# Optimization experiments

Hardware: AMD Instinct MI355X
Metric: run time of the kernel (lower is better)

## Reference

```python
import jax, jax.numpy as jnp
import numpy as np

K_PRED = 6
SCORE_TEMPERATURE = 0.5
NMS_THRESH = np.array([2.5, 1.0, 1.5], dtype=np.float32)  # [veh, ped, cyc] meters
SUPPRESSED_SCORE = 0.001


def setup_inputs() -> dict:
    key = jax.random.key(0)
    k0, k1, k2, k3 = jax.random.split(key, 4)
    D, S, A, P, T = 1, 64, 128, 6, 80  # n_decoder, n_scene, n_agent, n_pred, n_step_future
    pred_valid = jnp.ones((S, A), dtype=bool)
    pred_conf = jax.random.normal(k0, (D, S, A, P), dtype=jnp.float32)
    # scale positions to realistic meters so distances straddle the NMS thresholds
    pred_pos = jax.random.normal(k1, (D, S, A, P, T, 2), dtype=jnp.float32) * 10.0
    pred_yaw_bbox = jax.random.normal(k2, (D, S, A, P, T, 1), dtype=jnp.float32)
    type_idx = jax.random.randint(k3, (S, A), 0, 3)
    ref_type = jax.nn.one_hot(type_idx, 3, dtype=jnp.float32)
    return {
        'pred_valid': pred_valid,
        'pred_conf': pred_conf,
        'pred_pos': pred_pos,
        'pred_yaw_bbox': pred_yaw_bbox,
        'ref_type': ref_type,
    }


def _nms_one_agent(scores, within, valid):
    # scores: [K], within: [K, K] bool, valid: scalar bool
    order = jnp.argsort(-scores)  # descending, computed once on original scores

    def step(cur, k):
        # suppress k if any other prediction within distance has a (currently) higher score
        mask = within[k] & (cur > cur[k])
        new_val = jnp.where(jnp.any(mask), jnp.asarray(SUPPRESSED_SCORE, cur.dtype), cur[k])
        return cur.at[k].set(new_val), None

    out, _ = jax.lax.scan(step, scores, order)
    return jnp.where(valid, out, scores)


_nms = jax.vmap(jax.vmap(_nms_one_agent))  # over scene, agent


def reference(pred_valid, pred_conf, pred_pos, pred_yaw_bbox, ref_type):
    D, S, A, P, T, _ = pred_pos.shape
    K = D * P
    # [n_scene, n_agent, k_pred, n_step, 2]
    trajs = jnp.moveaxis(pred_pos, 0, 2).reshape(S, A, K, T, 2)
    scores = jax.nn.softmax(pred_conf, axis=-1)
    scores = jnp.moveaxis(scores, 0, 2).reshape(S, A, K)
    scores = scores / jnp.sum(scores, axis=-1, keepdims=True)

    # mpa_nms: per-agent-type distance threshold
    thresh = jnp.einsum('sat,t->sa', ref_type, jnp.asarray(NMS_THRESH))[:, :, None, None]
    # use_ade=True: mean pairwise distance over time -> [S, A, K, K]
    diff = trajs[:, :, :, None] - trajs[:, :, None, :]          # [S,A,K,K,T,2]
    within_dist = jnp.mean(jnp.linalg.norm(diff, axis=-1), axis=-1) < thresh
    scores = _nms(scores, within_dist, pred_valid)
    scores = scores / jnp.sum(scores, axis=-1, keepdims=True)

    # score temperature
    scores = jax.nn.softmax(jnp.log(scores) / SCORE_TEMPERATURE, axis=-1)

    waymo_trajs = jnp.moveaxis(trajs, 3, 1)                      # [S, T, A, K, 2]
    waymo_scores = scores                                        # [S, A, K]
    waymo_valid = jnp.broadcast_to(pred_valid[:, None, :], (S, T, A))
    yaw_bbox = jnp.moveaxis(pred_yaw_bbox, 0, 2).reshape(S, A, K, T, 1)
    waymo_yaw_bbox = jnp.moveaxis(yaw_bbox, 3, 1)                # [S, T, A, K, 1]
    return waymo_valid, waymo_trajs, waymo_scores, waymo_yaw_bbox
```

## Files before the change

### kernel.cpp

```cpp
#include <hip/hip_runtime.h>
#include <hip/hip_bf16.h>

#define NS 64
#define NA 128
#define NK 6
#define NT 80
#define THREADS 512
#define TILE_A 8
#define NROWS (TILE_A * NK)

#define OFF_TRAJ   655360
#define OFF_SCORE  (655360 + 7864320)
#define OFF_YAW    (655360 + 7864320 + 49152)

#define PSTRIDE 82
#define YSTRIDE 84

typedef float nfloat4 __attribute__((ext_vector_type(4)));

__global__ __launch_bounds__(THREADS) void waymo_post_kernel(
    const int*    __restrict__ validIn,
    const float*  __restrict__ confIn,
    const float2* __restrict__ posIn,
    const float*  __restrict__ yawIn,
    const float*  __restrict__ typeIn,
    float*        __restrict__ out)
{
    const int g   = blockIdx.x;
    const int tid = threadIdx.x;
    const int s   = g >> 4;
    const int a0  = (g & 15) * TILE_A;

    __shared__ float2 sPos[NROWS * PSTRIDE];
    __shared__ float  sYaw[NROWS * YSTRIDE];

    const size_t sa0 = (size_t)s * NA + a0;
    const float2* pbase = posIn + sa0 * (NK * NT);
    const float*  ybase = yawIn + sa0 * (NK * NT);

    for (int i = tid; i < NROWS * (NT / 2); i += THREADS) {
        int r = i / 40, q = i - r * 40;
        nfloat4 v = *(const nfloat4*)(pbase + (size_t)r * NT + 2 * q);
        *(nfloat4*)&sPos[r * PSTRIDE + 2 * q] = v;
    }
    for (int i = tid; i < NROWS * (NT / 4); i += THREADS) {
        int r = i / 20, m = i - r * 20;
        nfloat4 v = *(const nfloat4*)(ybase + (size_t)r * NT + 4 * m);
        *(nfloat4*)&sYaw[r * YSTRIDE + 4 * m] = v;
    }
    __syncthreads();

    float* outSc = out + OFF_SCORE;

    if (tid < 256) {
        const int la   = tid >> 5;
        const int lane = tid & 31;
        const int a    = a0 + la;
        const int p    = lane >> 1;
        const int half = lane & 1;

        const size_t sa = (size_t)s * NA + a;
        const float th = 2.5f * typeIn[sa * 3 + 0]
                       + 1.0f * typeIn[sa * 3 + 1]
                       + 1.5f * typeIn[sa * 3 + 2];

        int pi, pj;
        if      (p < 5)  { pi = 0; pj = p + 1; }
        else if (p < 9)  { pi = 1; pj = p - 3; }
        else if (p < 12) { pi = 2; pj = p - 6; }
        else if (p < 14) { pi = 3; pj = p - 8; }
        else             { pi = 4; pj = 5;     }

        const int rI = la * NK + pi, rJ = la * NK + pj;
        float dsum = 0.f;
        for (int t = half * 40; t < half * 40 + 40; ++t) {
            float2 u = sPos[rI * PSTRIDE + t];
            float2 v = sPos[rJ * PSTRIDE + t];
            float dx = u.x - v.x, dy = u.y - v.y;
            dsum += sqrtf(dx * dx + dy * dy);
        }
        dsum += __shfl_xor(dsum, 1);
        const bool within = (dsum / 80.0f) < th;
        const bool predb  = (half == 0) && (p < 15) && within;
        unsigned long long bal = __ballot(predb);
        unsigned mask32 = (unsigned)(bal >> (tid & 32));

        if (lane == 0) {
            float c[NK];
            float mx = -3e38f;
            for (int q = 0; q < NK; ++q) { c[q] = confIn[sa * NK + q]; mx = fmaxf(mx, c[q]); }
            float ssum = 0.f;
            for (int q = 0; q < NK; ++q) { c[q] = expf(c[q] - mx); ssum += c[q]; }
            for (int q = 0; q < NK; ++q) c[q] /= ssum;
            ssum = 0.f;
            for (int q = 0; q < NK; ++q) ssum += c[q];
            for (int q = 0; q < NK; ++q) c[q] /= ssum;

            int ord[NK]; bool used[NK];
            for (int q = 0; q < NK; ++q) used[q] = false;
            for (int st = 0; st < NK; ++st) {
                int best = 0; float bv = -3e38f;
                for (int q = 0; q < NK; ++q)
                    if (!used[q] && c[q] > bv) { bv = c[q]; best = q; }
                used[best] = true; ord[st] = best;
            }

            float cur[NK];
            for (int q = 0; q < NK; ++q) cur[q] = c[q];

            if (validIn[sa] != 0) {
                for (int st = 0; st < NK; ++st) {
                    int k = ord[st];
                    float ck = cur[k];
                    bool any = false;
                    for (int j = 0; j < NK; ++j) {
                        if (j == k) continue;
                        int lo = j < k ? j : k;
                        int hi = j < k ? k : j;
                        int pidx = lo * 5 - (lo * (lo - 1)) / 2 + (hi - lo - 1);
                        if (((mask32 >> (2 * pidx)) & 1u) && (cur[j] > ck)) any = true;
                    }
                    if (any) cur[k] = 0.001f;
                }
            }

            float tsum = 0.f;
            for (int q = 0; q < NK; ++q) tsum += cur[q];
            float w[NK]; float wsum = 0.f;
            for (int q = 0; q < NK; ++q) {
                float qq = cur[q] / tsum;
                w[q] = qq * qq; wsum += w[q];
            }
            for (int q = 0; q < NK; ++q) outSc[sa * NK + q] = w[q] / wsum;
        }
    }

    nfloat4* trajOut = (nfloat4*)(out + OFF_TRAJ);
    for (int o = tid; o < NT * 24; o += THREADS) {
        int t = o / 24, j = o - (o / 24) * 24;
        float2 u = sPos[(2 * j + 0) * PSTRIDE + t];
        float2 w = sPos[(2 * j + 1) * PSTRIDE + t];
        nfloat4 v{u.x, u.y, w.x, w.y};
        size_t f4 = (((size_t)(s * NT + t) * NA + a0) * NK) >> 1;
        __builtin_nontemporal_store(v, trajOut + f4 + j);
    }
    nfloat4* yawOut = (nfloat4*)(out + OFF_YAW);
    for (int o = tid; o < NT * 12; o += THREADS) {
        int t = o / 12, j = o - (o / 12) * 12;
        nfloat4 v{sYaw[(4 * j + 0) * YSTRIDE + t],
                  sYaw[(4 * j + 1) * YSTRIDE + t],
                  sYaw[(4 * j + 2) * YSTRIDE + t],
                  sYaw[(4 * j + 3) * YSTRIDE + t]};
        size_t f4 = (((size_t)(s * NT + t) * NA + a0) * NK) >> 2;
        __builtin_nontemporal_store(v, yawOut + f4 + j);
    }
    if (tid < 160) {
        int t = tid >> 1, q = tid & 1;
        nfloat4 v;
        v.x = (validIn[sa0 + 4 * q + 0] != 0) ? 1.0f : 0.0f;
        v.y = (validIn[sa0 + 4 * q + 1] != 0) ? 1.0f : 0.0f;
        v.z = (validIn[sa0 + 4 * q + 2] != 0) ? 1.0f : 0.0f;
        v.w = (validIn[sa0 + 4 * q + 3] != 0) ? 1.0f : 0.0f;
        size_t f4 = ((size_t)(s * NT + t) * NA + a0) >> 2;
        __builtin_nontemporal_store(v, (nfloat4*)out + f4 + q);
    }
}

extern "C" void kernel_launch(void* const* d_in, const int* in_sizes, int n_in,
                              void* d_out, int out_size, void* d_ws, size_t ws_size,
                              hipStream_t stream) {
    const int*    validIn = (const int*)d_in[0];
    const float*  confIn  = (const float*)d_in[1];
    const float2* posIn   = (const float2*)d_in[2];
    const float*  yawIn   = (const float*)d_in[3];
    const float*  typeIn  = (const float*)d_in[4];
    float* out = (float*)d_out;

    waymo_post_kernel<<<NS * (NA / TILE_A), THREADS, 0, stream>>>(
        validIn, confIn, posIn, yawIn, typeIn, out);
}
```

Before: 36.64 us.

## Split position and yaw work into separate specialized blocks with smaller tiles

The single block type that loaded both positions and yaw for 8 agents is replaced by two block roles. Two out of every three blocks handle positions, NMS and scores for 4 agents, and the third handles the yaw transpose and the valid mask for 8 agents, all with 256 threads. Each block needs less shared memory, there are more blocks overall, and loads use nontemporal hints, which should raise occupancy and spread the memory-bound transpose across more CUs. The odd LDS strides (81/85) are meant to reduce bank conflicts on the transposed reads, but the float4 stores into shared memory become scalar stores.

```diff
diff --git a/kernel.cpp b/kernel.cpp
--- a/kernel.cpp
+++ b/kernel.cpp
@@ -5,16 +5,21 @@
 #define NA 128
 #define NK 6
 #define NT 80
-#define THREADS 512
-#define TILE_A 8
-#define NROWS (TILE_A * NK)
+#define THREADS 256
 
 #define OFF_TRAJ   655360
 #define OFF_SCORE  (655360 + 7864320)
 #define OFF_YAW    (655360 + 7864320 + 49152)
 
-#define PSTRIDE 82
-#define YSTRIDE 84
+#define PA 4
+#define PROWS (PA * NK)
+#define PSTRIDE 81
+#define YA 8
+#define YROWS (YA * NK)
+#define YSTRIDE 85
+
+#define NPB (NS * (NA / PA))
+#define NYB (NS * (NA / YA))
 
 typedef float nfloat4 __attribute__((ext_vector_type(4)));
 
@@ -28,141 +33,161 @@
 {
     const int g   = blockIdx.x;
     const int tid = threadIdx.x;
-    const int s   = g >> 4;
-    const int a0  = (g & 15) * TILE_A;
-
-    __shared__ float2 sPos[NROWS * PSTRIDE];
-    __shared__ float  sYaw[NROWS * YSTRIDE];
-
-    const size_t sa0 = (size_t)s * NA + a0;
-    const float2* pbase = posIn + sa0 * (NK * NT);
-    const float*  ybase = yawIn + sa0 * (NK * NT);
-
-    for (int i = tid; i < NROWS * (NT / 2); i += THREADS) {
-        int r = i / 40, q = i - r * 40;
-        nfloat4 v = *(const nfloat4*)(pbase + (size_t)r * NT + 2 * q);
-        *(nfloat4*)&sPos[r * PSTRIDE + 2 * q] = v;
-    }
-    for (int i = tid; i < NROWS * (NT / 4); i += THREADS) {
-        int r = i / 20, m = i - r * 20;
-        nfloat4 v = *(const nfloat4*)(ybase + (size_t)r * NT + 4 * m);
-        *(nfloat4*)&sYaw[r * YSTRIDE + 4 * m] = v;
-    }
-    __syncthreads();
+
+    __shared__ float smem[YROWS * YSTRIDE];
 
     float* outSc = out + OFF_SCORE;
 
-    if (tid < 256) {
-        const int la   = tid >> 5;
-        const int lane = tid & 31;
-        const int a    = a0 + la;
-        const int p    = lane >> 1;
-        const int half = lane & 1;
-
-        const size_t sa = (size_t)s * NA + a;
-        const float th = 2.5f * typeIn[sa * 3 + 0]
-                       + 1.0f * typeIn[sa * 3 + 1]
-                       + 1.5f * typeIn[sa * 3 + 2];
-
-        int pi, pj;
-        if      (p < 5)  { pi = 0; pj = p + 1; }
-        else if (p < 9)  { pi = 1; pj = p - 3; }
-        else if (p < 12) { pi = 2; pj = p - 6; }
-        else if (p < 14) { pi = 3; pj = p - 8; }
-        else             { pi = 4; pj = 5;     }
-
-        const int rI = la * NK + pi, rJ = la * NK + pj;
-        float dsum = 0.f;
-        for (int t = half * 40; t < half * 40 + 40; ++t) {
-            float2 u = sPos[rI * PSTRIDE + t];
-            float2 v = sPos[rJ * PSTRIDE + t];
-            float dx = u.x - v.x, dy = u.y - v.y;
-            dsum += sqrtf(dx * dx + dy * dy);
-        }
-        dsum += __shfl_xor(dsum, 1);
-        const bool within = (dsum / 80.0f) < th;
-        const bool predb  = (half == 0) && (p < 15) && within;
-        unsigned long long bal = __ballot(predb);
-        unsigned mask32 = (unsigned)(bal >> (tid & 32));
-
-        if (lane == 0) {
-            float c[NK];
-            float mx = -3e38f;
-            for (int q = 0; q < NK; ++q) { c[q] = confIn[sa * NK + q]; mx = fmaxf(mx, c[q]); }
-            float ssum = 0.f;
-            for (int q = 0; q < NK; ++q) { c[q] = expf(c[q] - mx); ssum += c[q]; }
-            for (int q = 0; q < NK; ++q) c[q] /= ssum;
-            ssum = 0.f;
-            for (int q = 0; q < NK; ++q) ssum += c[q];
-            for (int q = 0; q < NK; ++q) c[q] /= ssum;
-
-            int ord[NK]; bool used[NK];
-            for (int q = 0; q < NK; ++q) used[q] = false;
-            for (int st = 0; st < NK; ++st) {
-                int best = 0; float bv = -3e38f;
-                for (int q = 0; q < NK; ++q)
-                    if (!used[q] && c[q] > bv) { bv = c[q]; best = q; }
-                used[best] = true; ord[st] = best;
+    const int e = g % 3;
+    if (e != 2) {
+        const int pb = (g / 3) * 2 + e;
+        const int s  = pb >> 5;
+        const int a0 = (pb & 31) * PA;
+
+        float2* P = (float2*)smem;
+        const size_t sa0 = (size_t)s * NA + a0;
+        const float2* pbase = posIn + sa0 * (NK * NT);
+
+        for (int i = tid; i < PROWS * (NT / 2); i += THREADS) {
+            int r = i / 40, q = i - r * 40;
+            nfloat4 v = __builtin_nontemporal_load((const nfloat4*)(pbase + (size_t)r * NT + 2 * q));
+            P[r * PSTRIDE + 2 * q + 0] = float2{v.x, v.y};
+            P[r * PSTRIDE + 2 * q + 1] = float2{v.z, v.w};
+        }
+        __syncthreads();
+
+        if (tid < 32 * PA) {
+            const int la   = tid >> 5;
+            const int lane = tid & 31;
+            const int a    = a0 + la;
+            const int p    = lane >> 1;
+            const int half = lane & 1;
+
+            const size_t sa = (size_t)s * NA + a;
+            const float th = 2.5f * typeIn[sa * 3 + 0]
+                           + 1.0f * typeIn[sa * 3 + 1]
+                           + 1.5f * typeIn[sa * 3 + 2];
+
+            int pi, pj;
+            if      (p < 5)  { pi = 0; pj = p + 1; }
+            else if (p < 9)  { pi = 1; pj = p - 3; }
+            else if (p < 12) { pi = 2; pj = p - 6; }
+            else if (p < 14) { pi = 3; pj = p - 8; }
+            else             { pi = 4; pj = 5;     }
+
+            const int rI = la * NK + pi, rJ = la * NK + pj;
+            float dsum = 0.f;
+            for (int t = half * 40; t < half * 40 + 40; ++t) {
+                float2 u = P[rI * PSTRIDE + t];
+                float2 v = P[rJ * PSTRIDE + t];
+                float dx = u.x - v.x, dy = u.y - v.y;
+                dsum += sqrtf(dx * dx + dy * dy);
             }
-
-            float cur[NK];
-            for (int q = 0; q < NK; ++q) cur[q] = c[q];
-
-            if (validIn[sa] != 0) {
+            dsum += __shfl_xor(dsum, 1);
+            const bool within = (dsum / 80.0f) < th;
+            const bool predb  = (half == 0) && (p < 15) && within;
+            unsigned long long bal = __ballot(predb);
+            unsigned mask32 = (unsigned)(bal >> (tid & 32));
+
+            if (lane == 0) {
+                float c[NK];
+                float mx = -3e38f;
+                for (int q = 0; q < NK; ++q) { c[q] = confIn[sa * NK + q]; mx = fmaxf(mx, c[q]); }
+                float ssum = 0.f;
+                for (int q = 0; q < NK; ++q) { c[q] = expf(c[q] - mx); ssum += c[q]; }
+                for (int q = 0; q < NK; ++q) c[q] /= ssum;
+                ssum = 0.f;
+                for (int q = 0; q < NK; ++q) ssum += c[q];
+                for (int q = 0; q < NK; ++q) c[q] /= ssum;
+
+                int ord[NK]; bool used[NK];
+                for (int q = 0; q < NK; ++q) used[q] = false;
                 for (int st = 0; st < NK; ++st) {
-                    int k = ord[st];
-                    float ck = cur[k];
-                    bool any = false;
-                    for (int j = 0; j < NK; ++j) {
-                        if (j == k) continue;
-                        int lo = j < k ? j : k;
-                        int hi = j < k ? k : j;
-                        int pidx = lo * 5 - (lo * (lo - 1)) / 2 + (hi - lo - 1);
-                        if (((mask32 >> (2 * pidx)) & 1u) && (cur[j] > ck)) any = true;
+                    int best = 0; float bv = -3e38f;
+                    for (int q = 0; q < NK; ++q)
+                        if (!used[q] && c[q] > bv) { bv = c[q]; best = q; }
+                    used[best] = true; ord[st] = best;
+                }
+
+                float cur[NK];
+                for (int q = 0; q < NK; ++q) cur[q] = c[q];
+
+                if (validIn[sa] != 0) {
+                    for (int st = 0; st < NK; ++st) {
+                        int k = ord[st];
+                        float ck = cur[k];
+                        bool any = false;
+                        for (int j = 0; j < NK; ++j) {
+                            if (j == k) continue;
+                            int lo = j < k ? j : k;
+                            int hi = j < k ? k : j;
+                            int pidx = lo * 5 - (lo * (lo - 1)) / 2 + (hi - lo - 1);
+                            if (((mask32 >> (2 * pidx)) & 1u) && (cur[j] > ck)) any = true;
+                        }
+                        if (any) cur[k] = 0.001f;
                     }
-                    if (any) cur[k] = 0.001f;
                 }
+
+                float tsum = 0.f;
+                for (int q = 0; q < NK; ++q) tsum += cur[q];
+                float w[NK]; float wsum = 0.f;
+                for (int q = 0; q < NK; ++q) {
+                    float qq = cur[q] / tsum;
+                    w[q] = qq * qq; wsum += w[q];
+                }
+                for (int q = 0; q < NK; ++q) outSc[sa * NK + q] = w[q] / wsum;
             }
-
-            float tsum = 0.f;
-            for (int q = 0; q < NK; ++q) tsum += cur[q];
-            float w[NK]; float wsum = 0.f;
-            for (int q = 0; q < NK; ++q) {
-                float qq = cur[q] / tsum;
-                w[q] = qq * qq; wsum += w[q];
-            }
-            for (int q = 0; q < NK; ++q) outSc[sa * NK + q] = w[q] / wsum;
-        }
-    }
-
-    nfloat4* trajOut = (nfloat4*)(out + OFF_TRAJ);
-    for (int o = tid; o < NT * 24; o += THREADS) {
-        int t = o / 24, j = o - (o / 24) * 24;
-        float2 u = sPos[(2 * j + 0) * PSTRIDE + t];
-        float2 w = sPos[(2 * j + 1) * PSTRIDE + t];
-        nfloat4 v{u.x, u.y, w.x, w.y};
-        size_t f4 = (((size_t)(s * NT + t) * NA + a0) * NK) >> 1;
-        __builtin_nontemporal_store(v, trajOut + f4 + j);
-    }
-    nfloat4* yawOut = (nfloat4*)(out + OFF_YAW);
-    for (int o = tid; o < NT * 12; o += THREADS) {
-        int t = o / 12, j = o - (o / 12) * 12;
-        nfloat4 v{sYaw[(4 * j + 0) * YSTRIDE + t],
-                  sYaw[(4 * j + 1) * YSTRIDE + t],
-                  sYaw[(4 * j + 2) * YSTRIDE + t],
-                  sYaw[(4 * j + 3) * YSTRIDE + t]};
-        size_t f4 = (((size_t)(s * NT + t) * NA + a0) * NK) >> 2;
-        __builtin_nontemporal_store(v, yawOut + f4 + j);
-    }
-    if (tid < 160) {
-        int t = tid >> 1, q = tid & 1;
-        nfloat4 v;
-        v.x = (validIn[sa0 + 4 * q + 0] != 0) ? 1.0f : 0.0f;
-        v.y = (validIn[sa0 + 4 * q + 1] != 0) ? 1.0f : 0.0f;
-        v.z = (validIn[sa0 + 4 * q + 2] != 0) ? 1.0f : 0.0f;
-        v.w = (validIn[sa0 + 4 * q + 3] != 0) ? 1.0f : 0.0f;
-        size_t f4 = ((size_t)(s * NT + t) * NA + a0) >> 2;
-        __builtin_nontemporal_store(v, (nfloat4*)out + f4 + q);
+        }
+
+        nfloat4* trajOut = (nfloat4*)(out + OFF_TRAJ);
+        for (int o = tid; o < NT * 12; o += THREADS) {
+            int t = o / 12, j = o - (o / 12) * 12;
+            float2 u = P[(2 * j + 0) * PSTRIDE + t];
+            float2 w = P[(2 * j + 1) * PSTRIDE + t];
+            nfloat4 v{u.x, u.y, w.x, w.y};
+            size_t f4 = (((size_t)(s * NT + t) * NA + a0) * NK) >> 1;
+            __builtin_nontemporal_store(v, trajOut + f4 + j);
+        }
+    } else {
+        const int yb = g / 3;
+        const int s  = yb >> 4;
+        const int a0 = (yb & 15) * YA;
+
+        float* Y = smem;
+        const size_t sa0 = (size_t)s * NA + a0;
+        const float* ybase = yawIn + sa0 * (NK * NT);
+
+        if (tid < 160) {
+            int t = tid >> 1, q = tid & 1;
+            nfloat4 v;
+            v.x = (validIn[sa0 + 4 * q + 0] != 0) ? 1.0f : 0.0f;
+            v.y = (validIn[sa0 + 4 * q + 1] != 0) ? 1.0f : 0.0f;
+            v.z = (validIn[sa0 + 4 * q + 2] != 0) ? 1.0f : 0.0f;
+            v.w = (validIn[sa0 + 4 * q + 3] != 0) ? 1.0f : 0.0f;
+            size_t f4 = ((size_t)(s * NT + t) * NA + a0) >> 2;
+            __builtin_nontemporal_store(v, (nfloat4*)out + f4 + q);
+        }
+
+        for (int i = tid; i < YROWS * (NT / 4); i += THREADS) {
+            int r = i / 20, m = i - r * 20;
+            nfloat4 v = __builtin_nontemporal_load((const nfloat4*)(ybase + (size_t)r * NT + 4 * m));
+            Y[r * YSTRIDE + 4 * m + 0] = v.x;
+            Y[r * YSTRIDE + 4 * m + 1] = v.y;
+            Y[r * YSTRIDE + 4 * m + 2] = v.z;
+            Y[r * YSTRIDE + 4 * m + 3] = v.w;
+        }
+        __syncthreads();
+
+        nfloat4* yawOut = (nfloat4*)(out + OFF_YAW);
+        for (int o = tid; o < NT * 12; o += THREADS) {
+            int t = o / 12, j = o - (o / 12) * 12;
+            nfloat4 v{Y[(4 * j + 0) * YSTRIDE + t],
+                      Y[(4 * j + 1) * YSTRIDE + t],
+                      Y[(4 * j + 2) * YSTRIDE + t],
+                      Y[(4 * j + 3) * YSTRIDE + t]};
+            size_t f4 = (((size_t)(s * NT + t) * NA + a0) * NK) >> 2;
+            __builtin_nontemporal_store(v, yawOut + f4 + j);
+        }
     }
 }
 
@@ -176,6 +201,6 @@
     const float*  typeIn  = (const float*)d_in[4];
     float* out = (float*)d_out;
 
-    waymo_post_kernel<<<NS * (NA / TILE_A), THREADS, 0, stream>>>(
+    waymo_post_kernel<<<NPB + NYB, THREADS, 0, stream>>>(
         validIn, confIn, posIn, yawIn, typeIn, out);
 }
```

After: 39.68 us. 8.3% more time.

## Transpose shared tiles to time-major and split NMS and output-writing warps

Applied to the files above, without the earlier changes.

Shared memory now holds positions and yaw time-major, so the transposed output writes become single vector LDS reads instead of strided gathers. Block size and agent tile are halved, which doubles the grid. Half the threads run the NMS/score path while the other half write the outputs concurrently, instead of every thread doing both one after the other. The cost is strided scalar LDS writes during the load phase and more blocks, each with less per-block parallelism for the copy.

```diff
diff --git a/kernel.cpp b/kernel.cpp
--- a/kernel.cpp
+++ b/kernel.cpp
@@ -5,16 +5,16 @@
 #define NA 128
 #define NK 6
 #define NT 80
-#define THREADS 512
-#define TILE_A 8
-#define NROWS (TILE_A * NK)
+#define THREADS 256
+#define TILE_A 4
+#define NR (TILE_A * NK)
 
 #define OFF_TRAJ   655360
 #define OFF_SCORE  (655360 + 7864320)
 #define OFF_YAW    (655360 + 7864320 + 49152)
 
-#define PSTRIDE 82
-#define YSTRIDE 84
+#define PS_T 26
+#define YS_T 28
 
 typedef float nfloat4 __attribute__((ext_vector_type(4)));
 
@@ -26,33 +26,34 @@
     const float*  __restrict__ typeIn,
     float*        __restrict__ out)
 {
-    const int g   = blockIdx.x;
+    const int s   = blockIdx.y;
+    const int a0  = blockIdx.x * TILE_A;
     const int tid = threadIdx.x;
-    const int s   = g >> 4;
-    const int a0  = (g & 15) * TILE_A;
 
-    __shared__ float2 sPos[NROWS * PSTRIDE];
-    __shared__ float  sYaw[NROWS * YSTRIDE];
+    __shared__ float2 sP[NT * PS_T];
+    __shared__ float  sY[NT * YS_T];
 
     const size_t sa0 = (size_t)s * NA + a0;
     const float2* pbase = posIn + sa0 * (NK * NT);
     const float*  ybase = yawIn + sa0 * (NK * NT);
 
-    for (int i = tid; i < NROWS * (NT / 2); i += THREADS) {
+    for (int i = tid; i < NR * (NT / 2); i += THREADS) {
         int r = i / 40, q = i - r * 40;
         nfloat4 v = *(const nfloat4*)(pbase + (size_t)r * NT + 2 * q);
-        *(nfloat4*)&sPos[r * PSTRIDE + 2 * q] = v;
+        sP[(2 * q + 0) * PS_T + r] = float2{v.x, v.y};
+        sP[(2 * q + 1) * PS_T + r] = float2{v.z, v.w};
     }
-    for (int i = tid; i < NROWS * (NT / 4); i += THREADS) {
+    for (int i = tid; i < NR * (NT / 4); i += THREADS) {
         int r = i / 20, m = i - r * 20;
         nfloat4 v = *(const nfloat4*)(ybase + (size_t)r * NT + 4 * m);
-        *(nfloat4*)&sYaw[r * YSTRIDE + 4 * m] = v;
+        sY[(4 * m + 0) * YS_T + r] = v.x;
+        sY[(4 * m + 1) * YS_T + r] = v.y;
+        sY[(4 * m + 2) * YS_T + r] = v.z;
+        sY[(4 * m + 3) * YS_T + r] = v.w;
     }
     __syncthreads();
 
-    float* outSc = out + OFF_SCORE;
-
-    if (tid < 256) {
+    if (tid < 32 * TILE_A) {
         const int la   = tid >> 5;
         const int lane = tid & 31;
         const int a    = a0 + la;
@@ -74,8 +75,8 @@
         const int rI = la * NK + pi, rJ = la * NK + pj;
         float dsum = 0.f;
         for (int t = half * 40; t < half * 40 + 40; ++t) {
-            float2 u = sPos[rI * PSTRIDE + t];
-            float2 v = sPos[rJ * PSTRIDE + t];
+            float2 u = sP[t * PS_T + rI];
+            float2 v = sP[t * PS_T + rJ];
             float dx = u.x - v.x, dy = u.y - v.y;
             dsum += sqrtf(dx * dx + dy * dy);
         }
@@ -131,38 +132,38 @@
                 float qq = cur[q] / tsum;
                 w[q] = qq * qq; wsum += w[q];
             }
+            float* outSc = out + OFF_SCORE;
             for (int q = 0; q < NK; ++q) outSc[sa * NK + q] = w[q] / wsum;
         }
-    }
+    } else {
+        const int o2 = tid - 128;
 
-    nfloat4* trajOut = (nfloat4*)(out + OFF_TRAJ);
-    for (int o = tid; o < NT * 24; o += THREADS) {
-        int t = o / 24, j = o - (o / 24) * 24;
-        float2 u = sPos[(2 * j + 0) * PSTRIDE + t];
-        float2 w = sPos[(2 * j + 1) * PSTRIDE + t];
-        nfloat4 v{u.x, u.y, w.x, w.y};
-        size_t f4 = (((size_t)(s * NT + t) * NA + a0) * NK) >> 1;
-        __builtin_nontemporal_store(v, trajOut + f4 + j);
-    }
-    nfloat4* yawOut = (nfloat4*)(out + OFF_YAW);
-    for (int o = tid; o < NT * 12; o += THREADS) {
-        int t = o / 12, j = o - (o / 12) * 12;
-        nfloat4 v{sYaw[(4 * j + 0) * YSTRIDE + t],
-                  sYaw[(4 * j + 1) * YSTRIDE + t],
-                  sYaw[(4 * j + 2) * YSTRIDE + t],
-                  sYaw[(4 * j + 3) * YSTRIDE + t]};
-        size_t f4 = (((size_t)(s * NT + t) * NA + a0) * NK) >> 2;
-        __builtin_nontemporal_store(v, yawOut + f4 + j);
-    }
-    if (tid < 160) {
-        int t = tid >> 1, q = tid & 1;
-        nfloat4 v;
-        v.x = (validIn[sa0 + 4 * q + 0] != 0) ? 1.0f : 0.0f;
-        v.y = (validIn[sa0 + 4 * q + 1] != 0) ? 1.0f : 0.0f;
-        v.z = (validIn[sa0 + 4 * q + 2] != 0) ? 1.0f : 0.0f;
-        v.w = (validIn[sa0 + 4 * q + 3] != 0) ? 1.0f : 0.0f;
-        size_t f4 = ((size_t)(s * NT + t) * NA + a0) >> 2;
-        __builtin_nontemporal_store(v, (nfloat4*)out + f4 + q);
+        if (o2 < NT) {
+            int t = o2;
+            nfloat4 v;
+            v.x = (validIn[sa0 + 0] != 0) ? 1.0f : 0.0f;
+            v.y = (validIn[sa0 + 1] != 0) ? 1.0f : 0.0f;
+            v.z = (validIn[sa0 + 2] != 0) ? 1.0f : 0.0f;
+            v.w = (validIn[sa0 + 3] != 0) ? 1.0f : 0.0f;
+            size_t f4 = (size_t)(s * NT + t) * (NA / 4) + (a0 >> 2);
+            __builtin_nontemporal_store(v, (nfloat4*)out + f4);
+        }
+
+        nfloat4* trajOut = (nfloat4*)(out + OFF_TRAJ);
+        for (int o = o2; o < NT * 12; o += 128) {
+            int t = o / 12, j = o - (o / 12) * 12;
+            nfloat4 v = *(const nfloat4*)&sP[t * PS_T + 2 * j];
+            size_t f4 = (size_t)(s * NT + t) * (NA * NK / 2) + a0 * 3 + j;
+            __builtin_nontemporal_store(v, trajOut + f4);
+        }
+
+        nfloat4* yawOut = (nfloat4*)(out + OFF_YAW);
+        for (int o = o2; o < NT * 6; o += 128) {
+            int t = o / 6, j = o - (o / 6) * 6;
+            nfloat4 v = *(const nfloat4*)&sY[t * YS_T + 4 * j];
+            size_t f4 = (size_t)(s * NT + t) * (NA * NK / 4) + ((a0 * 6) >> 2) + j;
+            __builtin_nontemporal_store(v, yawOut + f4);
+        }
     }
 }
 
@@ -176,6 +177,7 @@
     const float*  typeIn  = (const float*)d_in[4];
     float* out = (float*)d_out;
 
-    waymo_post_kernel<<<NS * (NA / TILE_A), THREADS, 0, stream>>>(
+    dim3 grid(NA / TILE_A, NS);
+    waymo_post_kernel<<<grid, THREADS, 0, stream>>>(
         validIn, confIn, posIn, yawIn, typeIn, out);
 }
```

Result: slower. 44.99 us (+22.8%).
